# Optimization experiments

Measured on AMD Instinct MI355X. Metric: run time of the kernel, lower is better.

The kernel has to match this reference:

```python
import jax, jax.numpy as jnp
import numpy as np

EMBED_DIM = 1024
NUM_HEADS = 16
HEAD_DIM = EMBED_DIM // NUM_HEADS
BATCH, SEQ = 1, 4096


def setup_inputs() -> dict:
    key = jax.random.key(0)
    k1, k2, k3 = jax.random.split(key, 3)
    hidden_states = jax.random.normal(k1, (BATCH, SEQ, EMBED_DIM), dtype=jnp.float32)
    W_qkv = jax.random.normal(k2, (3 * EMBED_DIM, EMBED_DIM), dtype=jnp.float32) * 0.02
    b_qkv = jnp.zeros((3 * EMBED_DIM,), dtype=jnp.float32)
    # torch init: identity per head, perturb slightly to make test non-trivial
    eye = jnp.broadcast_to(jnp.eye(HEAD_DIM, dtype=jnp.float32), (NUM_HEADS, HEAD_DIM, HEAD_DIM))
    hebbian_trace = eye + 0.01 * jax.random.normal(k3, (NUM_HEADS, HEAD_DIM, HEAD_DIM), dtype=jnp.float32)
    return {"hidden_states": hidden_states, "W_qkv": W_qkv, "b_qkv": b_qkv, "hebbian_trace": hebbian_trace}


def reference(hidden_states, W_qkv, b_qkv, hebbian_trace):
    B, S, E = hidden_states.shape
    H, D = NUM_HEADS, HEAD_DIM
    qkv = hidden_states @ W_qkv.T + b_qkv              # [B,S,3E]
    q, k, v = jnp.split(qkv, 3, axis=-1)
    # [B,H,S,D]
    q = q.reshape(B, S, H, D).transpose(0, 2, 1, 3)
    k = k.reshape(B, S, H, D).transpose(0, 2, 1, 3)
    v = v.reshape(B, S, H, D).transpose(0, 2, 1, 3)
    scores = jnp.einsum('bhqd,bhkd->bhqk', q, k) / jnp.sqrt(jnp.float32(D))
    attn = jax.nn.softmax(scores, axis=-1)
    weighted_v = jnp.einsum('bhqk,bhkd->bhqd', attn, v)  # [B,H,S,D]
    # torch einsum 'blhd,hdd->blhd': repeated 'd' in trace -> diagonal scaling
    wv = weighted_v.transpose(0, 2, 1, 3)               # [B,S,H,D]
    v_transformed = jnp.einsum('blhd,hdd->blhd', wv, hebbian_trace)
    return v_transformed.reshape(B, S, E)
```

## Files before the change

kernel.cpp:

```cpp
#include <hip/hip_runtime.h>
#include <hip/hip_bf16.h>
#include <stdint.h>

#define S_LEN 4096

typedef short s16x8  __attribute__((ext_vector_type(8)));
typedef float f32x4  __attribute__((ext_vector_type(4)));
typedef float f32x16 __attribute__((ext_vector_type(16)));

#define CEXP 0.18033688011112042f

__device__ __forceinline__ unsigned short f2bf(float f) {
    union { float f; unsigned u; } v; v.f = f;
    unsigned r = v.u + 0x7fffu + ((v.u >> 16) & 1u);
    return (unsigned short)(r >> 16);
}

__device__ __forceinline__ ushort2 pkbf(float a, float b) {
    float2 f; f.x = a; f.y = b;
    __hip_bfloat162 h = __float22bfloat162_rn(f);
    union { __hip_bfloat162 h; ushort2 u; } cv; cv.h = h;
    return cv.u;
}

__device__ __forceinline__ ushort4 pkbf4(float x, float y, float z, float w) {
    ushort2 lo = pkbf(x, y), hi = pkbf(z, w);
    ushort4 r; r.x = lo.x; r.y = lo.y; r.z = hi.x; r.w = hi.y;
    return r;
}

typedef const __attribute__((address_space(1))) void* gas_t;
typedef __attribute__((address_space(3))) void* sas_t;

__device__ __forceinline__ void async16(const void* g, void* s) {
    __builtin_amdgcn_global_load_lds((gas_t)g, (sas_t)s, 16, 0, 0);
}

__global__ __launch_bounds__(256) void cvt_bf16(
    const float* __restrict__ X, const float* __restrict__ W,
    unsigned short* __restrict__ Xb, unsigned short* __restrict__ Wb)
{
    const long NX = 4194304;
    long i = (long)(blockIdx.x * 256 + threadIdx.x) * 8;
    const float* src; unsigned short* dst; long off;
    if (i < NX) { src = X; dst = Xb; off = i; }
    else        { src = W; dst = Wb; off = i - NX; }
    float4 a = *(const float4*)(src + off);
    float4 b = *(const float4*)(src + off + 4);
    union { s16x8 v; ushort4 q[2]; } o;
    o.q[0] = pkbf4(a.x, a.y, a.z, a.w);
    o.q[1] = pkbf4(b.x, b.y, b.z, b.w);
    *(s16x8*)(dst + off) = o.v;
}

__global__ __launch_bounds__(256) void qkv_gemm_bf16(
    const unsigned short* __restrict__ Xb, const unsigned short* __restrict__ Wb,
    const float* __restrict__ bias, const float* __restrict__ trace,
    unsigned short* __restrict__ Qb, unsigned short* __restrict__ Kb,
    unsigned short* __restrict__ Vt)
{
    __shared__ __align__(16) unsigned short sm[17408];
    unsigned short* As = sm;
    unsigned short* Bs = sm + 8192;

    const int t = threadIdx.x;
    const int l = t & 63;
    const int w = t >> 6;
    const int bm = blockIdx.y, bn = blockIdx.x;
    const int rowBase = (w >> 1) * 64;
    const int colBase = (w & 1) * 64;

    f32x4 acc[4][4];
#pragma unroll
    for (int i = 0; i < 4; i++)
#pragma unroll
        for (int j = 0; j < 4; j++) acc[i][j] = (f32x4)0.f;

    const int srow = l >> 3;
    const int scol = (l & 7) * 8;

    for (int kt = 0; kt < 16; ++kt) {
        const int k0 = kt * 64;
#pragma unroll
        for (int c = 0; c < 4; ++c) {
            int m = w * 4 + c;
            const unsigned short* ga = Xb + (bm * 128 + m * 8 + srow) * 1024 + k0 + scol;
            const unsigned short* gb = Wb + (bn * 128 + m * 8 + srow) * 1024 + k0 + scol;
            async16(ga, As + m * 512);
            async16(gb, Bs + m * 512);
        }
        __syncthreads();

#pragma unroll
        for (int kc = 0; kc < 2; ++kc) {
            s16x8 af[4], bf[4];
#pragma unroll
            for (int i = 0; i < 4; i++) {
                af[i] = *(const s16x8*)(As + (rowBase + i * 16 + (l & 15)) * 64 + kc * 32 + (l >> 4) * 8);
                bf[i] = *(const s16x8*)(Bs + (colBase + i * 16 + (l & 15)) * 64 + kc * 32 + (l >> 4) * 8);
            }
#pragma unroll
            for (int i = 0; i < 4; i++)
#pragma unroll
                for (int j = 0; j < 4; j++)
                    acc[i][j] = __builtin_amdgcn_mfma_f32_16x16x32_bf16(af[i], bf[j], acc[i][j], 0, 0, 0);
        }
        __syncthreads();
    }

    if (bn < 16) {
#pragma unroll
        for (int j = 0; j < 4; j++) {
            int col = bn * 128 + colBase + j * 16 + (l & 15);
            float bv = bias[col];
            int region = col >> 10;
            int within = col & 1023;
            int h = within >> 6, d = within & 63;
            unsigned short* dst = (region == 0) ? Qb : Kb;
            float scl = (region == 0) ? CEXP : 1.0f;
#pragma unroll
            for (int i = 0; i < 4; i++) {
                int s0 = bm * 128 + rowBase + i * 16 + ((l >> 4) << 2);
#pragma unroll
                for (int r = 0; r < 4; r++)
                    dst[(h * S_LEN + s0 + r) * 64 + d] = f2bf((acc[i][j][r] + bv) * scl);
            }
        }
    } else {
        __syncthreads();
        unsigned short* Lt = sm;
#pragma unroll
        for (int j = 0; j < 4; j++) {
            int cl = colBase + j * 16 + (l & 15);
            int o  = bn * 128 + cl - 2048;
            float bv = bias[bn * 128 + cl];
            float tr = trace[(o >> 6) * 4096 + (o & 63) * 65];
#pragma unroll
            for (int i = 0; i < 4; i++) {
                int s0 = rowBase + i * 16 + ((l >> 4) << 2);
                *(ushort4*)(Lt + cl * 136 + s0) =
                    pkbf4((acc[i][j][0] + bv) * tr, (acc[i][j][1] + bv) * tr,
                          (acc[i][j][2] + bv) * tr, (acc[i][j][3] + bv) * tr);
            }
        }
        __syncthreads();
#pragma unroll
        for (int p = 0; p < 8; ++p) {
            int dl  = (t >> 4) + p * 16;
            int sch = (t & 15) * 8;
            int o = bn * 128 + dl - 2048;
            int h = o >> 6, d = o & 63;
            s16x8 v = *(const s16x8*)(Lt + dl * 136 + sch);
            *(s16x8*)(Vt + (h * 64 + d) * S_LEN + bm * 128 + sch) = v;
        }
    }
}

__global__ __launch_bounds__(256) void qkv_gemm_f32(
    const float* __restrict__ X, const float* __restrict__ W,
    const float* __restrict__ bias, const float* __restrict__ trace,
    unsigned short* __restrict__ Qb, unsigned short* __restrict__ Kb,
    unsigned short* __restrict__ Vt)
{
    __shared__ __align__(16) unsigned short sm[17408];
    unsigned short* As = sm;
    unsigned short* Bs = sm + 5120;

    const int t = threadIdx.x;
    const int l = t & 63;
    const int w = t >> 6;
    const int bm = blockIdx.y, bn = blockIdx.x;
    const int rowBase = (w >> 1) * 64;
    const int colBase = (w & 1) * 64;

    f32x4 acc[4][4];
#pragma unroll
    for (int i = 0; i < 4; i++)
#pragma unroll
        for (int j = 0; j < 4; j++) acc[i][j] = (f32x4)0.f;

    const int sr = t >> 3;
    const int sc = (t & 7) * 4;

    for (int kt = 0; kt < 32; ++kt) {
        const int k0 = kt * 32;
#pragma unroll
        for (int p = 0; p < 4; ++p) {
            int r = sr + p * 32;
            float4 xa = *(const float4*)(X + (bm * 128 + r) * 1024 + k0 + sc);
            float4 wb = *(const float4*)(W + (bn * 128 + r) * 1024 + k0 + sc);
            *(ushort4*)(As + r * 40 + sc) = pkbf4(xa.x, xa.y, xa.z, xa.w);
            *(ushort4*)(Bs + r * 40 + sc) = pkbf4(wb.x, wb.y, wb.z, wb.w);
        }
        __syncthreads();

        s16x8 af[4], bf[4];
#pragma unroll
        for (int i = 0; i < 4; i++) {
            af[i] = *(const s16x8*)(As + (rowBase + i * 16 + (l & 15)) * 40 + (l >> 4) * 8);
            bf[i] = *(const s16x8*)(Bs + (colBase + i * 16 + (l & 15)) * 40 + (l >> 4) * 8);
        }
#pragma unroll
        for (int i = 0; i < 4; i++)
#pragma unroll
            for (int j = 0; j < 4; j++)
                acc[i][j] = __builtin_amdgcn_mfma_f32_16x16x32_bf16(af[i], bf[j], acc[i][j], 0, 0, 0);
        __syncthreads();
    }

    if (bn < 16) {
#pragma unroll
        for (int j = 0; j < 4; j++) {
            int col = bn * 128 + colBase + j * 16 + (l & 15);
            float bv = bias[col];
            int region = col >> 10;
            int within = col & 1023;
            int h = within >> 6, d = within & 63;
            unsigned short* dst = (region == 0) ? Qb : Kb;
            float scl = (region == 0) ? CEXP : 1.0f;
#pragma unroll
            for (int i = 0; i < 4; i++) {
                int s0 = bm * 128 + rowBase + i * 16 + ((l >> 4) << 2);
#pragma unroll
                for (int r = 0; r < 4; r++)
                    dst[(h * S_LEN + s0 + r) * 64 + d] = f2bf((acc[i][j][r] + bv) * scl);
            }
        }
    } else {
        __syncthreads();
        unsigned short* Lt = sm;
#pragma unroll
        for (int j = 0; j < 4; j++) {
            int cl = colBase + j * 16 + (l & 15);
            int o  = bn * 128 + cl - 2048;
            float bv = bias[bn * 128 + cl];
            float tr = trace[(o >> 6) * 4096 + (o & 63) * 65];
#pragma unroll
            for (int i = 0; i < 4; i++) {
                int s0 = rowBase + i * 16 + ((l >> 4) << 2);
                *(ushort4*)(Lt + cl * 136 + s0) =
                    pkbf4((acc[i][j][0] + bv) * tr, (acc[i][j][1] + bv) * tr,
                          (acc[i][j][2] + bv) * tr, (acc[i][j][3] + bv) * tr);
            }
        }
        __syncthreads();
#pragma unroll
        for (int p = 0; p < 8; ++p) {
            int dl  = (t >> 4) + p * 16;
            int sch = (t & 15) * 8;
            int o = bn * 128 + dl - 2048;
            int h = o >> 6, d = o & 63;
            s16x8 v = *(const s16x8*)(Lt + dl * 136 + sch);
            *(s16x8*)(Vt + (h * 64 + d) * S_LEN + bm * 128 + sch) = v;
        }
    }
}

__global__ __launch_bounds__(512, 4) void attn(
    const unsigned short* __restrict__ Qb, const unsigned short* __restrict__ Kb,
    const unsigned short* __restrict__ Vt, float* __restrict__ out)
{
    __shared__ __align__(16) unsigned short sm[35840];
    __shared__ float lArr[256];

    const int t = threadIdx.x;
    const int l = t & 63;
    const int w = t >> 6;
    const int g = w >> 2;
    const int wq = w & 3;
    const int bid = blockIdx.x;
    const int xcd = bid & 7;
    const int j   = bid >> 3;
    const int h   = xcd * 2 + (j & 1);
    const int qblk = j >> 1;
    const int qbase = qblk * 128 + wq * 32;
    const int l31 = l & 31;
    const int lh  = l >> 5;

    unsigned short* Ks  = sm + g * 9216;
    unsigned short* Vts = sm + g * 9216 + 4608;
    unsigned short* Pw  = sm + 18432 + w * 2176 + l31 * 68;

    s16x8 qf[4];
#pragma unroll
    for (int ks = 0; ks < 4; ks++)
        qf[ks] = *(const s16x8*)(Qb + (h * S_LEN + qbase + l31) * 64 + ks * 16 + lh * 8);

    f32x16 O0 = (f32x16)0.f, O1 = (f32x16)0.f;
    float2 lpA; lpA.x = 0.f; lpA.y = 0.f;
    float2 lpB; lpB.x = 0.f; lpB.y = 0.f;

    const int tg    = t & 255;
    const int strow = tg >> 2;
    const int stch  = (tg & 3) * 16;

    for (int kt = 0; kt < 32; ++kt) {
        const int kv0 = g * 2048 + kt * 64;
        {
            const unsigned short* ksrc = Kb + (h * S_LEN + kv0 + strow) * 64 + stch;
            const unsigned short* vsrc = Vt + (h * 64 + strow) * S_LEN + kv0 + stch;
            s16x8 k0v = *(const s16x8*)(ksrc);
            s16x8 k1v = *(const s16x8*)(ksrc + 8);
            s16x8 v0v = *(const s16x8*)(vsrc);
            s16x8 v1v = *(const s16x8*)(vsrc + 8);
            *(s16x8*)(Ks  + strow * 72 + stch)     = k0v;
            *(s16x8*)(Ks  + strow * 72 + stch + 8) = k1v;
            *(s16x8*)(Vts + strow * 72 + stch)     = v0v;
            *(s16x8*)(Vts + strow * 72 + stch + 8) = v1v;
        }
        __syncthreads();

        f32x16 S0 = (f32x16)0.f, S1 = (f32x16)0.f;
#pragma unroll
        for (int ks = 0; ks < 4; ks++) {
            s16x8 a0 = *(const s16x8*)(Ks + l31 * 72 + ks * 16 + lh * 8);
            s16x8 a1 = *(const s16x8*)(Ks + (32 + l31) * 72 + ks * 16 + lh * 8);
            S0 = __builtin_amdgcn_mfma_f32_32x32x16_bf16(a0, qf[ks], S0, 0, 0, 0);
            S1 = __builtin_amdgcn_mfma_f32_32x32x16_bf16(a1, qf[ks], S1, 0, 0, 0);
        }

#pragma unroll
        for (int i = 0; i < 16; i += 4) {
            float p0 = __builtin_amdgcn_exp2f(S0[i+0]); S0[i+0] = p0; lpA.x += p0;
            float p1 = __builtin_amdgcn_exp2f(S0[i+1]); S0[i+1] = p1; lpA.y += p1;
            float p2 = __builtin_amdgcn_exp2f(S0[i+2]); S0[i+2] = p2; lpB.x += p2;
            float p3 = __builtin_amdgcn_exp2f(S0[i+3]); S0[i+3] = p3; lpB.y += p3;
        }
#pragma unroll
        for (int i = 0; i < 16; i += 4) {
            float p0 = __builtin_amdgcn_exp2f(S1[i+0]); S1[i+0] = p0; lpA.x += p0;
            float p1 = __builtin_amdgcn_exp2f(S1[i+1]); S1[i+1] = p1; lpA.y += p1;
            float p2 = __builtin_amdgcn_exp2f(S1[i+2]); S1[i+2] = p2; lpB.x += p2;
            float p3 = __builtin_amdgcn_exp2f(S1[i+3]); S1[i+3] = p3; lpB.y += p3;
        }

#pragma unroll
        for (int gq = 0; gq < 4; ++gq) {
            *(ushort4*)(Pw + gq * 8 + lh * 4)      = pkbf4(S0[gq*4], S0[gq*4+1], S0[gq*4+2], S0[gq*4+3]);
            *(ushort4*)(Pw + 32 + gq * 8 + lh * 4) = pkbf4(S1[gq*4], S1[gq*4+1], S1[gq*4+2], S1[gq*4+3]);
        }

#pragma unroll
        for (int ks = 0; ks < 4; ks++) {
            union { s16x8 v; ushort4 q[2]; } pu;
            pu.q[0] = *(const ushort4*)(Pw + ks * 16 + lh * 8);
            pu.q[1] = *(const ushort4*)(Pw + ks * 16 + lh * 8 + 4);
            s16x8 av0 = *(const s16x8*)(Vts + l31 * 72 + ks * 16 + lh * 8);
            s16x8 av1 = *(const s16x8*)(Vts + (32 + l31) * 72 + ks * 16 + lh * 8);
            O0 = __builtin_amdgcn_mfma_f32_32x32x16_bf16(av0, pu.v, O0, 0, 0, 0);
            O1 = __builtin_amdgcn_mfma_f32_32x32x16_bf16(av1, pu.v, O1, 0, 0, 0);
        }
        __syncthreads();
    }

    float l_part = (lpA.x + lpA.y) + (lpB.x + lpB.y);
    float l_tot = l_part + __shfl_xor(l_part, 32);
    if (lh == 0) lArr[w * 32 + l31] = l_tot;

    float* Lo = (float*)sm + w * 2176;
#pragma unroll
    for (int dt = 0; dt < 2; ++dt) {
        const f32x16& Ox = dt ? O1 : O0;
#pragma unroll
        for (int gq = 0; gq < 4; ++gq) {
            int d0 = dt * 32 + gq * 8 + lh * 4;
            float4 vv;
            vv.x = Ox[gq*4+0]; vv.y = Ox[gq*4+1]; vv.z = Ox[gq*4+2]; vv.w = Ox[gq*4+3];
            *(float4*)(Lo + l31 * 68 + d0) = vv;
        }
    }
    __syncthreads();

    if (w < 4) {
        const float* LoA = (float*)sm + w * 2176;
        const float* LoB = (float*)sm + (w + 4) * 2176;
#pragma unroll
        for (int it = 0; it < 8; ++it) {
            int ql = it * 4 + (l >> 4);
            float invl = 1.0f / (lArr[w * 32 + ql] + lArr[(w + 4) * 32 + ql]);
            float4 a = *(const float4*)(LoA + ql * 68 + (l & 15) * 4);
            float4 b = *(const float4*)(LoB + ql * 68 + (l & 15) * 4);
            float4 vv;
            vv.x = (a.x + b.x) * invl;
            vv.y = (a.y + b.y) * invl;
            vv.z = (a.z + b.z) * invl;
            vv.w = (a.w + b.w) * invl;
            *(float4*)(out + (qblk * 128 + w * 32 + ql) * 1024 + h * 64 + (l & 15) * 4) = vv;
        }
    }
}

extern "C" void kernel_launch(void* const* d_in, const int* in_sizes, int n_in,
                              void* d_out, int out_size, void* d_ws, size_t ws_size,
                              hipStream_t stream) {
    const float* X     = (const float*)d_in[0];
    const float* W     = (const float*)d_in[1];
    const float* bias  = (const float*)d_in[2];
    const float* trace = (const float*)d_in[3];
    float* out = (float*)d_out;

    unsigned short* Qb = (unsigned short*)d_ws;
    unsigned short* Kb = Qb + 4194304;
    unsigned short* Vt = Kb + 4194304;
    unsigned short* Xb = Vt + 4194304;
    unsigned short* Wb = Xb + 4194304;

    const size_t NEED_BF16 = (size_t)3 * 8388608 + 8388608 + 6291456;

    if (ws_size >= NEED_BF16) {
        cvt_bf16<<<3584, 256, 0, stream>>>(X, W, Xb, Wb);
        qkv_gemm_bf16<<<dim3(24, 32), 256, 0, stream>>>(Xb, Wb, bias, trace, Qb, Kb, Vt);
    } else {
        qkv_gemm_f32<<<dim3(24, 32), 256, 0, stream>>>(X, W, bias, trace, Qb, Kb, Vt);
    }
    attn<<<512, 512, 0, stream>>>(Qb, Kb, Vt, out);
}
```

Baseline: 212.7 us.

## Double-buffer K/V tiles via register prefetch and pass P through permlane swaps

Result: slower. 284.4 us (+33.7%).

```diff
diff --git a/kernel.cpp b/kernel.cpp
--- a/kernel.cpp
+++ b/kernel.cpp
@@ -27,6 +27,10 @@
     ushort2 lo = pkbf(x, y), hi = pkbf(z, w);
     ushort4 r; r.x = lo.x; r.y = lo.y; r.z = hi.x; r.w = hi.y;
     return r;
+}
+
+__device__ __forceinline__ unsigned pku(float a, float b) {
+    union { ushort2 s; unsigned u; } c; c.s = pkbf(a, b); return c.u;
 }
 
 typedef const __attribute__((address_space(1))) void* gas_t;
@@ -260,7 +264,7 @@
     const unsigned short* __restrict__ Qb, const unsigned short* __restrict__ Kb,
     const unsigned short* __restrict__ Vt, float* __restrict__ out)
 {
-    __shared__ __align__(16) unsigned short sm[35840];
+    __shared__ __align__(16) unsigned short sm[36864];
     __shared__ float lArr[256];
 
     const int t = threadIdx.x;
@@ -277,10 +281,6 @@
     const int l31 = l & 31;
     const int lh  = l >> 5;
 
-    unsigned short* Ks  = sm + g * 9216;
-    unsigned short* Vts = sm + g * 9216 + 4608;
-    unsigned short* Pw  = sm + 18432 + w * 2176 + l31 * 68;
-
     s16x8 qf[4];
 #pragma unroll
     for (int ks = 0; ks < 4; ks++)
@@ -294,23 +294,38 @@
     const int strow = tg >> 2;
     const int stch  = (tg & 3) * 16;
 
+    const unsigned short* kp = Kb + (h * S_LEN + g * 2048 + strow) * 64 + stch;
+    const unsigned short* vp = Vt + (h * 64 + strow) * S_LEN + g * 2048 + stch;
+
+    s16x8 rk0 = *(const s16x8*)(kp);
+    s16x8 rk1 = *(const s16x8*)(kp + 8);
+    s16x8 rv0 = *(const s16x8*)(vp);
+    s16x8 rv1 = *(const s16x8*)(vp + 8);
+    {
+        unsigned short* K0 = sm + g * 9216;
+        *(s16x8*)(K0 + strow * 72 + stch)          = rk0;
+        *(s16x8*)(K0 + strow * 72 + stch + 8)      = rk1;
+        *(s16x8*)(K0 + 4608 + strow * 72 + stch)     = rv0;
+        *(s16x8*)(K0 + 4608 + strow * 72 + stch + 8) = rv1;
+    }
+
     for (int kt = 0; kt < 32; ++kt) {
-        const int kv0 = g * 2048 + kt * 64;
-        {
-            const unsigned short* ksrc = Kb + (h * S_LEN + kv0 + strow) * 64 + stch;
-            const unsigned short* vsrc = Vt + (h * 64 + strow) * S_LEN + kv0 + stch;
-            s16x8 k0v = *(const s16x8*)(ksrc);
-            s16x8 k1v = *(const s16x8*)(ksrc + 8);
-            s16x8 v0v = *(const s16x8*)(vsrc);
-            s16x8 v1v = *(const s16x8*)(vsrc + 8);
-            *(s16x8*)(Ks  + strow * 72 + stch)     = k0v;
-            *(s16x8*)(Ks  + strow * 72 + stch + 8) = k1v;
-            *(s16x8*)(Vts + strow * 72 + stch)     = v0v;
-            *(s16x8*)(Vts + strow * 72 + stch + 8) = v1v;
-        }
-        __syncthreads();
+        __syncthreads();
+        const int cur = kt & 1;
+        unsigned short* Ks  = sm + (cur * 2 + g) * 9216;
+        unsigned short* Vts = Ks + 4608;
+
+        if (kt < 31) {
+            kp += 4096;
+            vp += 64;
+            rk0 = *(const s16x8*)(kp);
+            rk1 = *(const s16x8*)(kp + 8);
+            rv0 = *(const s16x8*)(vp);
+            rv1 = *(const s16x8*)(vp + 8);
+        }
 
         f32x16 S0 = (f32x16)0.f, S1 = (f32x16)0.f;
+        __builtin_amdgcn_s_setprio(1);
 #pragma unroll
         for (int ks = 0; ks < 4; ks++) {
             s16x8 a0 = *(const s16x8*)(Ks + l31 * 72 + ks * 16 + lh * 8);
@@ -318,6 +333,7 @@
             S0 = __builtin_amdgcn_mfma_f32_32x32x16_bf16(a0, qf[ks], S0, 0, 0, 0);
             S1 = __builtin_amdgcn_mfma_f32_32x32x16_bf16(a1, qf[ks], S1, 0, 0, 0);
         }
+        __builtin_amdgcn_s_setprio(0);
 
 #pragma unroll
         for (int i = 0; i < 16; i += 4) {
@@ -334,28 +350,40 @@
             float p3 = __builtin_amdgcn_exp2f(S1[i+3]); S1[i+3] = p3; lpB.y += p3;
         }
 
-#pragma unroll
-        for (int gq = 0; gq < 4; ++gq) {
-            *(ushort4*)(Pw + gq * 8 + lh * 4)      = pkbf4(S0[gq*4], S0[gq*4+1], S0[gq*4+2], S0[gq*4+3]);
-            *(ushort4*)(Pw + 32 + gq * 8 + lh * 4) = pkbf4(S1[gq*4], S1[gq*4+1], S1[gq*4+2], S1[gq*4+3]);
-        }
-
+        __builtin_amdgcn_s_setprio(1);
 #pragma unroll
         for (int ks = 0; ks < 4; ks++) {
-            union { s16x8 v; ushort4 q[2]; } pu;
-            pu.q[0] = *(const ushort4*)(Pw + ks * 16 + lh * 8);
-            pu.q[1] = *(const ushort4*)(Pw + ks * 16 + lh * 8 + 4);
+            const f32x16 Sx = (ks < 2) ? S0 : S1;
+            const int b = (ks & 1) * 8;
+            unsigned pa0 = pku(Sx[b+0], Sx[b+1]);
+            unsigned pc0 = pku(Sx[b+4], Sx[b+5]);
+            unsigned pa1 = pku(Sx[b+2], Sx[b+3]);
+            unsigned pc1 = pku(Sx[b+6], Sx[b+7]);
+            auto r0 = __builtin_amdgcn_permlane32_swap(pa0, pc0, false, false);
+            auto r1 = __builtin_amdgcn_permlane32_swap(pa1, pc1, false, false);
+            union { s16x8 v; unsigned u[4]; } pb;
+            pb.u[0] = r0[0]; pb.u[1] = r1[0]; pb.u[2] = r0[1]; pb.u[3] = r1[1];
             s16x8 av0 = *(const s16x8*)(Vts + l31 * 72 + ks * 16 + lh * 8);
             s16x8 av1 = *(const s16x8*)(Vts + (32 + l31) * 72 + ks * 16 + lh * 8);
-            O0 = __builtin_amdgcn_mfma_f32_32x32x16_bf16(av0, pu.v, O0, 0, 0, 0);
-            O1 = __builtin_amdgcn_mfma_f32_32x32x16_bf16(av1, pu.v, O1, 0, 0, 0);
-        }
-        __syncthreads();
+            O0 = __builtin_amdgcn_mfma_f32_32x32x16_bf16(av0, pb.v, O0, 0, 0, 0);
+            O1 = __builtin_amdgcn_mfma_f32_32x32x16_bf16(av1, pb.v, O1, 0, 0, 0);
+        }
+        __builtin_amdgcn_s_setprio(0);
+
+        if (kt < 31) {
+            unsigned short* Kn = sm + (((cur ^ 1) * 2) + g) * 9216;
+            *(s16x8*)(Kn + strow * 72 + stch)          = rk0;
+            *(s16x8*)(Kn + strow * 72 + stch + 8)      = rk1;
+            *(s16x8*)(Kn + 4608 + strow * 72 + stch)     = rv0;
+            *(s16x8*)(Kn + 4608 + strow * 72 + stch + 8) = rv1;
+        }
     }
 
     float l_part = (lpA.x + lpA.y) + (lpB.x + lpB.y);
     float l_tot = l_part + __shfl_xor(l_part, 32);
     if (lh == 0) lArr[w * 32 + l31] = l_tot;
+
+    __syncthreads();
 
     float* Lo = (float*)sm + w * 2176;
 #pragma unroll
```

## Double-buffer K/V tiles with async LDS loads and register-based P transpose

Applied to the files above, without the earlier changes.

New measurement: 208.3 us. -2.1%, faster.

```diff
diff --git a/kernel.cpp b/kernel.cpp
--- a/kernel.cpp
+++ b/kernel.cpp
@@ -27,6 +27,10 @@
     ushort2 lo = pkbf(x, y), hi = pkbf(z, w);
     ushort4 r; r.x = lo.x; r.y = lo.y; r.z = hi.x; r.w = hi.y;
     return r;
+}
+
+__device__ __forceinline__ unsigned pku(float a, float b) {
+    union { ushort2 s; unsigned u; } c; c.s = pkbf(a, b); return c.u;
 }
 
 typedef const __attribute__((address_space(1))) void* gas_t;
@@ -260,13 +264,14 @@
     const unsigned short* __restrict__ Qb, const unsigned short* __restrict__ Kb,
     const unsigned short* __restrict__ Vt, float* __restrict__ out)
 {
-    __shared__ __align__(16) unsigned short sm[35840];
+    __shared__ __align__(16) unsigned short sm[34816];
     __shared__ float lArr[256];
 
     const int t = threadIdx.x;
     const int l = t & 63;
     const int w = t >> 6;
     const int g = w >> 2;
+    const int wg = w & 3;
     const int wq = w & 3;
     const int bid = blockIdx.x;
     const int xcd = bid & 7;
@@ -276,10 +281,7 @@
     const int qbase = qblk * 128 + wq * 32;
     const int l31 = l & 31;
     const int lh  = l >> 5;
-
-    unsigned short* Ks  = sm + g * 9216;
-    unsigned short* Vts = sm + g * 9216 + 4608;
-    unsigned short* Pw  = sm + 18432 + w * 2176 + l31 * 68;
+    const int swz = l31 & 7;
 
     s16x8 qf[4];
 #pragma unroll
@@ -290,72 +292,93 @@
     float2 lpA; lpA.x = 0.f; lpA.y = 0.f;
     float2 lpB; lpB.x = 0.f; lpB.y = 0.f;
 
-    const int tg    = t & 255;
-    const int strow = tg >> 2;
-    const int stch  = (tg & 3) * 16;
+    const int p0 = (wg * 2 + 0) * 64 + l;
+    const int p1 = (wg * 2 + 1) * 64 + l;
+    const int r0_ = p0 >> 3, c0_ = (p0 & 7) ^ (r0_ & 7);
+    const int r1_ = p1 >> 3, c1_ = (p1 & 7) ^ (r1_ & 7);
+    const unsigned short* gk0 = Kb + (h * S_LEN + g * 2048 + r0_) * 64 + c0_ * 8;
+    const unsigned short* gk1 = Kb + (h * S_LEN + g * 2048 + r1_) * 64 + c1_ * 8;
+    const unsigned short* gv0 = Vt + (h * 64 + r0_) * S_LEN + g * 2048 + c0_ * 8;
+    const unsigned short* gv1 = Vt + (h * 64 + r1_) * S_LEN + g * 2048 + c1_ * 8;
+
+    {
+        unsigned short* kb_ = sm + g * 8192 + wg * 1024;
+        async16(gk0, kb_);
+        async16(gk1, kb_ + 512);
+        async16(gv0, kb_ + 4096);
+        async16(gv1, kb_ + 4096 + 512);
+    }
 
     for (int kt = 0; kt < 32; ++kt) {
-        const int kv0 = g * 2048 + kt * 64;
-        {
-            const unsigned short* ksrc = Kb + (h * S_LEN + kv0 + strow) * 64 + stch;
-            const unsigned short* vsrc = Vt + (h * 64 + strow) * S_LEN + kv0 + stch;
-            s16x8 k0v = *(const s16x8*)(ksrc);
-            s16x8 k1v = *(const s16x8*)(ksrc + 8);
-            s16x8 v0v = *(const s16x8*)(vsrc);
-            s16x8 v1v = *(const s16x8*)(vsrc + 8);
-            *(s16x8*)(Ks  + strow * 72 + stch)     = k0v;
-            *(s16x8*)(Ks  + strow * 72 + stch + 8) = k1v;
-            *(s16x8*)(Vts + strow * 72 + stch)     = v0v;
-            *(s16x8*)(Vts + strow * 72 + stch + 8) = v1v;
-        }
-        __syncthreads();
+        __syncthreads();
+        const unsigned short* sb  = sm + ((kt & 1) * 2 + g) * 8192;
+        const unsigned short* vbs = sb + 4096;
+
+        if (kt < 31) {
+            gk0 += 4096; gk1 += 4096; gv0 += 64; gv1 += 64;
+            unsigned short* kb_ = sm + (((kt + 1) & 1) * 2 + g) * 8192 + wg * 1024;
+            async16(gk0, kb_);
+            async16(gk1, kb_ + 512);
+            async16(gv0, kb_ + 4096);
+            async16(gv1, kb_ + 4096 + 512);
+        }
 
         f32x16 S0 = (f32x16)0.f, S1 = (f32x16)0.f;
+        __builtin_amdgcn_s_setprio(1);
 #pragma unroll
         for (int ks = 0; ks < 4; ks++) {
-            s16x8 a0 = *(const s16x8*)(Ks + l31 * 72 + ks * 16 + lh * 8);
-            s16x8 a1 = *(const s16x8*)(Ks + (32 + l31) * 72 + ks * 16 + lh * 8);
+            const int off = ((ks * 2 + lh) ^ swz) * 8;
+            s16x8 a0 = *(const s16x8*)(sb + l31 * 64 + off);
+            s16x8 a1 = *(const s16x8*)(sb + (32 + l31) * 64 + off);
             S0 = __builtin_amdgcn_mfma_f32_32x32x16_bf16(a0, qf[ks], S0, 0, 0, 0);
             S1 = __builtin_amdgcn_mfma_f32_32x32x16_bf16(a1, qf[ks], S1, 0, 0, 0);
         }
+        __builtin_amdgcn_s_setprio(0);
 
 #pragma unroll
         for (int i = 0; i < 16; i += 4) {
-            float p0 = __builtin_amdgcn_exp2f(S0[i+0]); S0[i+0] = p0; lpA.x += p0;
-            float p1 = __builtin_amdgcn_exp2f(S0[i+1]); S0[i+1] = p1; lpA.y += p1;
-            float p2 = __builtin_amdgcn_exp2f(S0[i+2]); S0[i+2] = p2; lpB.x += p2;
-            float p3 = __builtin_amdgcn_exp2f(S0[i+3]); S0[i+3] = p3; lpB.y += p3;
+            float p0v = __builtin_amdgcn_exp2f(S0[i+0]); S0[i+0] = p0v; lpA.x += p0v;
+            float p1v = __builtin_amdgcn_exp2f(S0[i+1]); S0[i+1] = p1v; lpA.y += p1v;
+            float p2v = __builtin_amdgcn_exp2f(S0[i+2]); S0[i+2] = p2v; lpB.x += p2v;
+            float p3v = __builtin_amdgcn_exp2f(S0[i+3]); S0[i+3] = p3v; lpB.y += p3v;
         }
 #pragma unroll
         for (int i = 0; i < 16; i += 4) {
-            float p0 = __builtin_amdgcn_exp2f(S1[i+0]); S1[i+0] = p0; lpA.x += p0;
-            float p1 = __builtin_amdgcn_exp2f(S1[i+1]); S1[i+1] = p1; lpA.y += p1;
-            float p2 = __builtin_amdgcn_exp2f(S1[i+2]); S1[i+2] = p2; lpB.x += p2;
-            float p3 = __builtin_amdgcn_exp2f(S1[i+3]); S1[i+3] = p3; lpB.y += p3;
-        }
-
-#pragma unroll
-        for (int gq = 0; gq < 4; ++gq) {
-            *(ushort4*)(Pw + gq * 8 + lh * 4)      = pkbf4(S0[gq*4], S0[gq*4+1], S0[gq*4+2], S0[gq*4+3]);
-            *(ushort4*)(Pw + 32 + gq * 8 + lh * 4) = pkbf4(S1[gq*4], S1[gq*4+1], S1[gq*4+2], S1[gq*4+3]);
-        }
-
-#pragma unroll
-        for (int ks = 0; ks < 4; ks++) {
-            union { s16x8 v; ushort4 q[2]; } pu;
-            pu.q[0] = *(const ushort4*)(Pw + ks * 16 + lh * 8);
-            pu.q[1] = *(const ushort4*)(Pw + ks * 16 + lh * 8 + 4);
-            s16x8 av0 = *(const s16x8*)(Vts + l31 * 72 + ks * 16 + lh * 8);
-            s16x8 av1 = *(const s16x8*)(Vts + (32 + l31) * 72 + ks * 16 + lh * 8);
-            O0 = __builtin_amdgcn_mfma_f32_32x32x16_bf16(av0, pu.v, O0, 0, 0, 0);
-            O1 = __builtin_amdgcn_mfma_f32_32x32x16_bf16(av1, pu.v, O1, 0, 0, 0);
-        }
-        __syncthreads();
+            float p0v = __builtin_amdgcn_exp2f(S1[i+0]); S1[i+0] = p0v; lpA.x += p0v;
+            float p1v = __builtin_amdgcn_exp2f(S1[i+1]); S1[i+1] = p1v; lpA.y += p1v;
+            float p2v = __builtin_amdgcn_exp2f(S1[i+2]); S1[i+2] = p2v; lpB.x += p2v;
+            float p3v = __builtin_amdgcn_exp2f(S1[i+3]); S1[i+3] = p3v; lpB.y += p3v;
+        }
+
+        __builtin_amdgcn_s_setprio(1);
+#define PVBLK(SX, BO, KS) do {                                               \
+        unsigned pa0 = pku(SX[(BO)+0], SX[(BO)+1]);                          \
+        unsigned pc0 = pku(SX[(BO)+4], SX[(BO)+5]);                          \
+        unsigned pa1 = pku(SX[(BO)+2], SX[(BO)+3]);                          \
+        unsigned pc1 = pku(SX[(BO)+6], SX[(BO)+7]);                          \
+        auto r0 = __builtin_amdgcn_permlane32_swap(pa0, pc0, false, false);  \
+        auto r1 = __builtin_amdgcn_permlane32_swap(pa1, pc1, false, false);  \
+        union { s16x8 v; unsigned u[4]; } pb_;                               \
+        pb_.u[0] = r0[0]; pb_.u[1] = r1[0]; pb_.u[2] = r0[1]; pb_.u[3] = r1[1]; \
+        const int offv = (((KS) * 2 + lh) ^ swz) * 8;                        \
+        s16x8 av0 = *(const s16x8*)(vbs + l31 * 64 + offv);                  \
+        s16x8 av1 = *(const s16x8*)(vbs + (32 + l31) * 64 + offv);           \
+        O0 = __builtin_amdgcn_mfma_f32_32x32x16_bf16(av0, pb_.v, O0, 0, 0, 0); \
+        O1 = __builtin_amdgcn_mfma_f32_32x32x16_bf16(av1, pb_.v, O1, 0, 0, 0); \
+    } while (0)
+        PVBLK(S0, 0, 0);
+        PVBLK(S0, 8, 1);
+        PVBLK(S1, 0, 2);
+        PVBLK(S1, 8, 3);
+#undef PVBLK
+        __builtin_amdgcn_s_setprio(0);
     }
 
     float l_part = (lpA.x + lpA.y) + (lpB.x + lpB.y);
     float l_tot = l_part + __shfl_xor(l_part, 32);
     if (lh == 0) lArr[w * 32 + l31] = l_tot;
+
+    __syncthreads();
 
     float* Lo = (float*)sm + w * 2176;
 #pragma unroll
```
